# Optimization experiments

Measured on AMD Instinct MI355X. Metric: run time of the kernel, lower is better.

## Reference

```python
import jax, jax.numpy as jnp
import numpy as np

B, S, D = 2, 2048, 1024
E, H = 8, 2816  # hidden = 256*ceil(int(2*(4*1024)/3)/256) = 2816
TOP_K = 2


def setup_inputs() -> dict:
    key = jax.random.key(0)
    k0, k1, k2, k3, k4 = jax.random.split(key, 5)
    x = jax.random.normal(k0, (B, S, D), dtype=jnp.float32)
    wg = jax.random.normal(k1, (D, E), dtype=jnp.float32) * (D ** -0.5)
    w1 = jax.random.normal(k2, (E, D, H), dtype=jnp.float32) * 0.02  # gate proj
    w3 = jax.random.normal(k3, (E, D, H), dtype=jnp.float32) * 0.02  # up proj
    w2 = jax.random.normal(k4, (E, H, D), dtype=jnp.float32) * 0.02  # down proj
    return {"x": x, "wg": wg, "w1": w1, "w2": w2, "w3": w3}


def reference(x, wg, w1, w2, w3):
    Bb, Ss, Dd = x.shape
    Ee = w1.shape[0]
    xf = x.reshape(-1, Dd)                       # [T, D]
    logits = xf @ wg                              # [T, E]
    probs = jax.nn.softmax(logits, axis=-1)
    topk_p, topk_i = jax.lax.top_k(probs, TOP_K)  # [T, K]
    topk_p = topk_p / jnp.sum(topk_p, axis=-1, keepdims=True)
    # combine weight per (token, expert): sum over top-k slots
    cw = jnp.sum(jax.nn.one_hot(topk_i, Ee, dtype=xf.dtype) * topk_p[..., None], axis=1)  # [T, E]
    out = jnp.zeros_like(xf)
    for e in range(Ee):  # fixed small loop over experts
        h = jax.nn.silu(xf @ w1[e]) * (xf @ w3[e])   # [T, H] SwiGLU
        out = out + cw[:, e:e + 1] * (h @ w2[e])     # weighted combine
    return out.reshape(Bb, Ss, Dd)
```

## Files before the change

### kernel.cpp

```cpp
#include <hip/hip_runtime.h>
#include <hip/hip_bf16.h>

typedef unsigned short u16;
typedef __bf16 bf16_t;
typedef bf16_t bf16x8 __attribute__((ext_vector_type(8)));
typedef float f32x4 __attribute__((ext_vector_type(4)));

#define T_TOK 4096
#define DIM   1024
#define NEXP  8
#define HID   2816
#define CAP   16
#define DBUF  (128*32)

static __device__ __forceinline__ u16 f2b(float f) {
    __hip_bfloat16 h = __float2bfloat16(f);
    return *(u16*)&h;
}

static __device__ __forceinline__ void glds16(const u16* g, u16* l) {
    __builtin_amdgcn_global_load_lds((const __attribute__((address_space(1))) void*)g,
                                     (__attribute__((address_space(3))) void*)l, 16, 0, 0);
}

__global__ void k_gating(const float* __restrict__ X,
                         const float* __restrict__ WG,
                         int* __restrict__ cnt,
                         int* __restrict__ tok,
                         float* __restrict__ wt,
                         u16* __restrict__ Xbf)
{
    int wv   = threadIdx.x >> 6;
    int lane = threadIdx.x & 63;
    int t = blockIdx.x * 4 + wv;
    float l[NEXP];
#pragma unroll
    for (int e = 0; e < NEXP; ++e) l[e] = 0.f;
#pragma unroll
    for (int i = 0; i < DIM/64; ++i) {
        int d = i*64 + lane;
        float xv = X[(size_t)t*DIM + d];
        Xbf[(size_t)t*DIM + d] = f2b(xv);
        const float* wrow = WG + (size_t)d*NEXP;
        float4 wa = *(const float4*)wrow;
        float4 wb = *(const float4*)(wrow + 4);
        l[0] += xv*wa.x; l[1] += xv*wa.y; l[2] += xv*wa.z; l[3] += xv*wa.w;
        l[4] += xv*wb.x; l[5] += xv*wb.y; l[6] += xv*wb.z; l[7] += xv*wb.w;
    }
#pragma unroll
    for (int e = 0; e < NEXP; ++e) {
#pragma unroll
        for (int s = 32; s > 0; s >>= 1)
            l[e] += __shfl_xor(l[e], s, 64);
    }
    if (lane == 0) {
        int i1 = 0; float b1 = l[0];
#pragma unroll
        for (int e = 1; e < NEXP; ++e) if (l[e] > b1) { b1 = l[e]; i1 = e; }
        int i2 = -1; float b2 = 0.f;
#pragma unroll
        for (int e = 0; e < NEXP; ++e) {
            if (e == i1) continue;
            if (i2 < 0 || l[e] > b2) { b2 = l[e]; i2 = e; }
        }
        float p1 = 1.f / (1.f + __expf(b2 - b1));
        float p2 = 1.f - p1;
        int pos = atomicAdd(&cnt[i1], 1);
        tok[i1*T_TOK + pos] = t;  wt[i1*T_TOK + pos] = p1;
        pos = atomicAdd(&cnt[i2], 1);
        tok[i2*T_TOK + pos] = t;  wt[i2*T_TOK + pos] = p2;
    }
}

__global__ void k_compact(const int* __restrict__ cnt,
                          const int* __restrict__ tok, const float* __restrict__ wt,
                          int* __restrict__ ctok, float* __restrict__ cwt)
{
    int e = blockIdx.x;
    int off = 0;
    for (int i = 0; i < e; ++i) off += cnt[i];
    int n = cnt[e];
    for (int i = threadIdx.x; i < n; i += blockDim.x) {
        ctok[off + i] = tok[e*T_TOK + i];
        cwt [off + i] = wt [e*T_TOK + i];
    }
}

#define TS 72
__global__ void k_transpose_cast(const float* __restrict__ in, u16* __restrict__ out,
                                 int R, int C)
{
    __shared__ u16 tle[64*TS];
    size_t mb = (size_t)blockIdx.z * (size_t)R * C;
    int r0 = blockIdx.x * 64, c0 = blockIdx.y * 64;
    int tid = threadIdx.x;
    const float* I = in + mb + (size_t)r0*C + c0;
#pragma unroll
    for (int p = 0; p < 4; ++p) {
        int q = tid + p*256;
        int r = q >> 4, cc = (q & 15) * 4;
        float4 v = *(const float4*)&I[(size_t)r*C + cc];
        tle[(cc+0)*TS + r] = f2b(v.x);
        tle[(cc+1)*TS + r] = f2b(v.y);
        tle[(cc+2)*TS + r] = f2b(v.z);
        tle[(cc+3)*TS + r] = f2b(v.w);
    }
    __syncthreads();
    u16* O = out + mb + (size_t)c0*R + r0;
    int rc = tid & 7, oc = tid >> 3;
#pragma unroll
    for (int p = 0; p < 2; ++p) {
        int c = oc + p*32;
        *(uint4*)&O[(size_t)c*R + rc*8] = *(const uint4*)&tle[c*TS + rc*8];
    }
}

__global__ __launch_bounds__(256, 3) void k_gemm1(
    const u16* __restrict__ X, const u16* __restrict__ W1t, const u16* __restrict__ W3t,
    u16* __restrict__ Hbuf, const int* __restrict__ cnt, const int* __restrict__ ctok)
{
    __shared__ u16 As[2*DBUF];
    __shared__ u16 Bs[2*DBUF];
    __shared__ int tokLds[128];

    const int bid = blockIdx.x;
    const int e   = bid & 7;
    const int q   = bid >> 3;
    const int mt0 = q & (CAP-1);
    const int col = q >> 4;
    const int ne  = cnt[e];
    const int ntile = (ne + 127) >> 7;
    if (mt0 >= ntile) return;
    int off = 0;
    for (int i = 0; i < e; ++i) off += cnt[i];
    const int h0 = col * 64;

    const int tid = threadIdx.x, wave = tid >> 6, lane = tid & 63;
    const int wr = wave >> 1, wc = wave & 1;
    const int quad = lane >> 4, lr = lane & 15;
    const int lrow = lane >> 2;
    const int swk  = ((lane & 3) ^ ((lane >> 3) & 3)) * 8;
    const int jx   = (quad ^ ((lr >> 1) & 3)) * 8;

    const size_t wb = (size_t)e * HID * DIM;
    const u16* w1g = W1t + wb + (size_t)(h0 + wave*16 + lrow)*DIM + swk;
    const u16* w3g = W3t + wb + (size_t)(h0 + wave*16 + lrow)*DIM + swk;
    u16* aL0 = &As[(wave*16)*32];
    u16* aL1 = &As[(64 + wave*16)*32];
    u16* bL0 = &Bs[(wave*16)*32];
    u16* bL1 = &Bs[(64 + wave*16)*32];

#define G1_STAGE(K, OFS)              \
    glds16(ag0 + (K), aL0 + (OFS));   \
    glds16(ag1 + (K), aL1 + (OFS));   \
    glds16(w1g + (K), bL0 + (OFS));   \
    glds16(w3g + (K), bL1 + (OFS));

#define G1_COMPUTE(OFS)                                                             \
    {                                                                               \
        bf16x8 af[4], b1[2], b3[2];                                                 \
        _Pragma("unroll")                                                           \
        for (int m = 0; m < 4; ++m)                                                 \
            af[m] = *(const bf16x8*)&As[(OFS) + (wr*64 + m*16 + lr)*32 + jx];       \
        _Pragma("unroll")                                                           \
        for (int n = 0; n < 2; ++n) {                                               \
            b1[n] = *(const bf16x8*)&Bs[(OFS) + (wc*32 + n*16 + lr)*32 + jx];       \
            b3[n] = *(const bf16x8*)&Bs[(OFS) + (64 + wc*32 + n*16 + lr)*32 + jx];  \
        }                                                                           \
        __builtin_amdgcn_s_setprio(1);                                              \
        _Pragma("unroll")                                                           \
        for (int m = 0; m < 4; ++m)                                                 \
            _Pragma("unroll")                                                       \
            for (int n = 0; n < 2; ++n) {                                           \
                a1[m][n] = __builtin_amdgcn_mfma_f32_16x16x32_bf16(af[m], b1[n], a1[m][n], 0, 0, 0); \
                a3[m][n] = __builtin_amdgcn_mfma_f32_16x16x32_bf16(af[m], b3[n], a3[m][n], 0, 0, 0); \
            }                                                                       \
        __builtin_amdgcn_s_setprio(0);                                              \
    }

    for (int tile = mt0; tile < ntile; tile += CAP) {
        const int m0 = tile << 7;
        int nvalid = ne - m0; if (nvalid > 128) nvalid = 128;

        __syncthreads();
        if (tid < 128) {
            int i = (tid < nvalid) ? tid : (nvalid - 1);
            tokLds[tid] = ctok[off + m0 + i];
        }
        __syncthreads();
        const u16* ag0 = X + (size_t)tokLds[wave*16 + lrow]*DIM + swk;
        const u16* ag1 = X + (size_t)tokLds[64 + wave*16 + lrow]*DIM + swk;

        f32x4 a1[4][2], a3[4][2];
#pragma unroll
        for (int m = 0; m < 4; ++m)
#pragma unroll
            for (int n = 0; n < 2; ++n) {
                a1[m][n] = (f32x4){0.f,0.f,0.f,0.f};
                a3[m][n] = (f32x4){0.f,0.f,0.f,0.f};
            }

        G1_STAGE(0, 0)

        for (int k0 = 0; k0 < DIM; k0 += 64) {
            G1_STAGE(k0 + 32, DBUF)
            asm volatile("s_waitcnt vmcnt(4)" ::: "memory");
            __builtin_amdgcn_s_barrier();
            G1_COMPUTE(0)
            asm volatile("s_waitcnt lgkmcnt(0)" ::: "memory");
            __builtin_amdgcn_s_barrier();
            if (k0 + 64 < DIM) {
                G1_STAGE(k0 + 64, 0)
                asm volatile("s_waitcnt vmcnt(4)" ::: "memory");
            } else {
                asm volatile("s_waitcnt vmcnt(0)" ::: "memory");
            }
            __builtin_amdgcn_s_barrier();
            G1_COMPUTE(DBUF)
            asm volatile("s_waitcnt lgkmcnt(0)" ::: "memory");
            __builtin_amdgcn_s_barrier();
        }

#pragma unroll
        for (int m = 0; m < 4; ++m) {
            int mb_ = wr*64 + m*16 + quad*4;
#pragma unroll
            for (int rr = 0; rr < 4; ++rr) {
                int mm = mb_ + rr;
                if (mm >= nvalid) continue;
                u16* hrow = Hbuf + (size_t)(off + m0 + mm)*HID + h0 + wc*32 + lr;
#pragma unroll
                for (int n = 0; n < 2; ++n) {
                    float g = a1[m][n][rr];
                    float u = a3[m][n][rr];
                    hrow[n*16] = f2b((g / (1.f + __expf(-g))) * u);
                }
            }
        }
    }
#undef G1_STAGE
#undef G1_COMPUTE
}

__global__ __launch_bounds__(256, 3) void k_gemm2(
    const u16* __restrict__ Hbuf, const u16* __restrict__ W2t,
    float* __restrict__ outf, const int* __restrict__ cnt,
    const int* __restrict__ ctok, const float* __restrict__ cwt)
{
    __shared__ u16 As[2*DBUF];
    __shared__ u16 Bs[2*DBUF];
    __shared__ int   tLds[128];
    __shared__ float wLds[128];

    const int bid = blockIdx.x;
    const int e   = bid & 7;
    const int q   = bid >> 3;
    const int mt0 = q & (CAP-1);
    const int r2  = q >> 4;
    const int zk  = r2 & 1;
    const int d0  = (r2 >> 1) * 128;
    const int ne  = cnt[e];
    const int ntile = (ne + 127) >> 7;
    if (mt0 >= ntile) return;
    int off = 0;
    for (int i = 0; i < e; ++i) off += cnt[i];
    const int kb = zk * (HID/2);

    const int tid = threadIdx.x, wave = tid >> 6, lane = tid & 63;
    const int wr = wave >> 1, wc = wave & 1;
    const int quad = lane >> 4, lr = lane & 15;
    const int lrow = lane >> 2;
    const int swk  = ((lane & 3) ^ ((lane >> 3) & 3)) * 8;
    const int jx   = (quad ^ ((lr >> 1) & 3)) * 8;

    const size_t w2b = (size_t)e * DIM * HID;
    const u16* bg0 = W2t + w2b + (size_t)(d0 + wave*16 + lrow)*HID + kb + swk;
    const u16* bg1 = bg0 + (size_t)64*HID;
    u16* aL0 = &As[(wave*16)*32];
    u16* aL1 = &As[(64 + wave*16)*32];
    u16* bL0 = &Bs[(wave*16)*32];
    u16* bL1 = &Bs[(64 + wave*16)*32];

#define G2_STAGE(K, OFS)              \
    glds16(ag0 + (K), aL0 + (OFS));   \
    glds16(ag1 + (K), aL1 + (OFS));   \
    glds16(bg0 + (K), bL0 + (OFS));   \
    glds16(bg1 + (K), bL1 + (OFS));

#define G2_COMPUTE(OFS)                                                             \
    {                                                                               \
        bf16x8 af[4], bb[4];                                                        \
        _Pragma("unroll")                                                           \
        for (int m = 0; m < 4; ++m)                                                 \
            af[m] = *(const bf16x8*)&As[(OFS) + (wr*64 + m*16 + lr)*32 + jx];       \
        _Pragma("unroll")                                                           \
        for (int n = 0; n < 4; ++n)                                                 \
            bb[n] = *(const bf16x8*)&Bs[(OFS) + (wc*64 + n*16 + lr)*32 + jx];       \
        __builtin_amdgcn_s_setprio(1);                                              \
        _Pragma("unroll")                                                           \
        for (int m = 0; m < 4; ++m)                                                 \
            _Pragma("unroll")                                                       \
            for (int n = 0; n < 4; ++n)                                             \
                acc[m][n] = __builtin_amdgcn_mfma_f32_16x16x32_bf16(af[m], bb[n], acc[m][n], 0, 0, 0); \
        __builtin_amdgcn_s_setprio(0);                                              \
    }

    for (int tile = mt0; tile < ntile; tile += CAP) {
        const int m0 = tile << 7;
        int nvalid = ne - m0; if (nvalid > 128) nvalid = 128;

        __syncthreads();
        if (tid < 128) {
            int i = (tid < nvalid) ? tid : (nvalid - 1);
            tLds[tid] = ctok[off + m0 + i];
            wLds[tid] = cwt [off + m0 + i];
        }
        __syncthreads();
        int ar0 = wave*16 + lrow;      if (ar0 >= nvalid) ar0 = nvalid - 1;
        int ar1 = 64 + wave*16 + lrow; if (ar1 >= nvalid) ar1 = nvalid - 1;
        const u16* ag0 = Hbuf + (size_t)(off + m0 + ar0)*HID + kb + swk;
        const u16* ag1 = Hbuf + (size_t)(off + m0 + ar1)*HID + kb + swk;

        f32x4 acc[4][4];
#pragma unroll
        for (int a = 0; a < 4; ++a)
#pragma unroll
            for (int b = 0; b < 4; ++b) acc[a][b] = (f32x4){0.f,0.f,0.f,0.f};

        G2_STAGE(0, 0)

        for (int k0 = 0; k0 < HID/2; k0 += 64) {
            G2_STAGE(k0 + 32, DBUF)
            asm volatile("s_waitcnt vmcnt(4)" ::: "memory");
            __builtin_amdgcn_s_barrier();
            G2_COMPUTE(0)
            asm volatile("s_waitcnt lgkmcnt(0)" ::: "memory");
            __builtin_amdgcn_s_barrier();
            if (k0 + 64 < HID/2) {
                G2_STAGE(k0 + 64, 0)
                asm volatile("s_waitcnt vmcnt(4)" ::: "memory");
            } else {
                asm volatile("s_waitcnt vmcnt(0)" ::: "memory");
            }
            __builtin_amdgcn_s_barrier();
            G2_COMPUTE(DBUF)
            asm volatile("s_waitcnt lgkmcnt(0)" ::: "memory");
            __builtin_amdgcn_s_barrier();
        }

#pragma unroll
        for (int m = 0; m < 4; ++m) {
            int mb_ = wr*64 + m*16 + quad*4;
#pragma unroll
            for (int rr = 0; rr < 4; ++rr) {
                int mm = mb_ + rr;
                if (mm >= nvalid) continue;
                float wr_ = wLds[mm];
                float* orow = outf + (size_t)tLds[mm]*DIM + d0 + wc*64 + lr;
#pragma unroll
                for (int n = 0; n < 4; ++n)
                    atomicAdd(&orow[n*16], acc[m][n][rr] * wr_);
            }
        }
    }
#undef G2_STAGE
#undef G2_COMPUTE
}

extern "C" void kernel_launch(void* const* d_in, const int* in_sizes, int n_in,
                              void* d_out, int out_size, void* d_ws, size_t ws_size,
                              hipStream_t stream)
{
    const float* x  = (const float*)d_in[0];
    const float* wg = (const float*)d_in[1];
    const float* w1 = (const float*)d_in[2];
    const float* w2 = (const float*)d_in[3];
    const float* w3 = (const float*)d_in[4];
    float* outf = (float*)d_out;

    char* ws = (char*)d_ws;
    int*   cnt  = (int*)  (ws);
    int*   tok  = (int*)  (ws + 256);
    float* wt   = (float*)(ws + 131328);
    int*   ctok = (int*)  (ws + 262400);
    float* cwt  = (float*)(ws + 295168);
    u16*   Xbf  = (u16*)  (ws + 327936);
    u16*   Hbuf = (u16*)  (ws + 8716544);
    u16*   W1t  = (u16*)  (ws + 54853888);
    u16*   W3t  = (u16*)  (ws + 100991232);
    u16*   W2t  = (u16*)  (ws + 147128576);

    hipMemsetAsync(cnt, 0, 256, stream);
    hipMemsetAsync(outf, 0, (size_t)T_TOK*DIM*sizeof(float), stream);

    k_transpose_cast<<<dim3(DIM/64, HID/64, NEXP), 256, 0, stream>>>(w1, W1t, DIM, HID);
    k_transpose_cast<<<dim3(DIM/64, HID/64, NEXP), 256, 0, stream>>>(w3, W3t, DIM, HID);
    k_transpose_cast<<<dim3(HID/64, DIM/64, NEXP), 256, 0, stream>>>(w2, W2t, HID, DIM);

    k_gating<<<T_TOK/4, 256, 0, stream>>>(x, wg, cnt, tok, wt, Xbf);
    k_compact<<<NEXP, 256, 0, stream>>>(cnt, tok, wt, ctok, cwt);

    k_gemm1<<<NEXP*(HID/64)*CAP, 256, 0, stream>>>(Xbf, W1t, W3t, Hbuf, cnt, ctok);
    k_gemm2<<<NEXP*CAP*2*(DIM/128), 256, 0, stream>>>(Hbuf, W2t, outf, cnt, ctok, cwt);
}
```

Measured before the change: 663.8 us.

## Deepen GEMM LDS pipeline to four stages and swizzle transpose LDS

Both expert GEMM kernels move from a 2-slot double buffer to a 4-slot ring that keeps three K-slices of async global->LDS loads in flight, with explicit vmcnt waits and a drained epilogue. This is meant to hide more global memory latency behind the MFMA work. The cost is twice the LDS per block, so launch bounds drop from 3 to 2 blocks per CU, which lowers occupancy. The transpose-cast kernel also gets an XOR swizzle on its LDS tile to cut bank conflicts.

```diff
diff --git a/kernel.cpp b/kernel.cpp
--- a/kernel.cpp
+++ b/kernel.cpp
@@ -99,11 +99,12 @@
     for (int p = 0; p < 4; ++p) {
         int q = tid + p*256;
         int r = q >> 4, cc = (q & 15) * 4;
+        int rw = r ^ ((q & 7) << 3);
         float4 v = *(const float4*)&I[(size_t)r*C + cc];
-        tle[(cc+0)*TS + r] = f2b(v.x);
-        tle[(cc+1)*TS + r] = f2b(v.y);
-        tle[(cc+2)*TS + r] = f2b(v.z);
-        tle[(cc+3)*TS + r] = f2b(v.w);
+        tle[(cc+0)*TS + rw] = f2b(v.x);
+        tle[(cc+1)*TS + rw] = f2b(v.y);
+        tle[(cc+2)*TS + rw] = f2b(v.z);
+        tle[(cc+3)*TS + rw] = f2b(v.w);
     }
     __syncthreads();
     u16* O = out + mb + (size_t)c0*R + r0;
@@ -111,16 +112,17 @@
 #pragma unroll
     for (int p = 0; p < 2; ++p) {
         int c = oc + p*32;
-        *(uint4*)&O[(size_t)c*R + rc*8] = *(const uint4*)&tle[c*TS + rc*8];
-    }
-}
-
-__global__ __launch_bounds__(256, 3) void k_gemm1(
+        int rs = rc ^ ((c >> 2) & 7);
+        *(uint4*)&O[(size_t)c*R + rc*8] = *(const uint4*)&tle[c*TS + rs*8];
+    }
+}
+
+__global__ __launch_bounds__(256, 2) void k_gemm1(
     const u16* __restrict__ X, const u16* __restrict__ W1t, const u16* __restrict__ W3t,
     u16* __restrict__ Hbuf, const int* __restrict__ cnt, const int* __restrict__ ctok)
 {
-    __shared__ u16 As[2*DBUF];
-    __shared__ u16 Bs[2*DBUF];
+    __shared__ u16 As[4*DBUF];
+    __shared__ u16 Bs[4*DBUF];
     __shared__ int tokLds[128];
 
     const int bid = blockIdx.x;
@@ -150,11 +152,12 @@
     u16* bL0 = &Bs[(wave*16)*32];
     u16* bL1 = &Bs[(64 + wave*16)*32];
 
-#define G1_STAGE(K, OFS)              \
-    glds16(ag0 + (K), aL0 + (OFS));   \
-    glds16(ag1 + (K), aL1 + (OFS));   \
-    glds16(w1g + (K), bL0 + (OFS));   \
-    glds16(w3g + (K), bL1 + (OFS));
+#define G1_STAGE(S, SLOT)                         \
+    {   int _k = (S)*32;                          \
+        glds16(ag0 + _k, aL0 + (SLOT)*DBUF);      \
+        glds16(ag1 + _k, aL1 + (SLOT)*DBUF);      \
+        glds16(w1g + _k, bL0 + (SLOT)*DBUF);      \
+        glds16(w3g + _k, bL1 + (SLOT)*DBUF);  }
 
 #define G1_COMPUTE(OFS)                                                             \
     {                                                                               \
@@ -201,25 +204,42 @@
             }
 
         G1_STAGE(0, 0)
-
-        for (int k0 = 0; k0 < DIM; k0 += 64) {
-            G1_STAGE(k0 + 32, DBUF)
-            asm volatile("s_waitcnt vmcnt(4)" ::: "memory");
-            __builtin_amdgcn_s_barrier();
-            G1_COMPUTE(0)
-            asm volatile("s_waitcnt lgkmcnt(0)" ::: "memory");
-            __builtin_amdgcn_s_barrier();
-            if (k0 + 64 < DIM) {
-                G1_STAGE(k0 + 64, 0)
-                asm volatile("s_waitcnt vmcnt(4)" ::: "memory");
-            } else {
-                asm volatile("s_waitcnt vmcnt(0)" ::: "memory");
+        G1_STAGE(1, 1)
+        G1_STAGE(2, 2)
+
+        for (int j = 0; j < 32/4 - 1; ++j) {
+#pragma unroll
+            for (int t = 0; t < 4; ++t) {
+                const int i = 4*j + t;
+                G1_STAGE(i + 3, (t + 3) & 3)
+                asm volatile("s_waitcnt vmcnt(12)" ::: "memory");
+                __builtin_amdgcn_s_barrier();
+                G1_COMPUTE(t*DBUF)
+                asm volatile("s_waitcnt lgkmcnt(0)" ::: "memory");
+                __builtin_amdgcn_s_barrier();
             }
-            __builtin_amdgcn_s_barrier();
-            G1_COMPUTE(DBUF)
-            asm volatile("s_waitcnt lgkmcnt(0)" ::: "memory");
-            __builtin_amdgcn_s_barrier();
-        }
+        }
+        G1_STAGE(31, 3)
+        asm volatile("s_waitcnt vmcnt(12)" ::: "memory");
+        __builtin_amdgcn_s_barrier();
+        G1_COMPUTE(0*DBUF)
+        asm volatile("s_waitcnt lgkmcnt(0)" ::: "memory");
+        __builtin_amdgcn_s_barrier();
+        asm volatile("s_waitcnt vmcnt(8)" ::: "memory");
+        __builtin_amdgcn_s_barrier();
+        G1_COMPUTE(1*DBUF)
+        asm volatile("s_waitcnt lgkmcnt(0)" ::: "memory");
+        __builtin_amdgcn_s_barrier();
+        asm volatile("s_waitcnt vmcnt(4)" ::: "memory");
+        __builtin_amdgcn_s_barrier();
+        G1_COMPUTE(2*DBUF)
+        asm volatile("s_waitcnt lgkmcnt(0)" ::: "memory");
+        __builtin_amdgcn_s_barrier();
+        asm volatile("s_waitcnt vmcnt(0)" ::: "memory");
+        __builtin_amdgcn_s_barrier();
+        G1_COMPUTE(3*DBUF)
+        asm volatile("s_waitcnt lgkmcnt(0)" ::: "memory");
+        __builtin_amdgcn_s_barrier();
 
 #pragma unroll
         for (int m = 0; m < 4; ++m) {
@@ -242,13 +262,13 @@
 #undef G1_COMPUTE
 }
 
-__global__ __launch_bounds__(256, 3) void k_gemm2(
+__global__ __launch_bounds__(256, 2) void k_gemm2(
     const u16* __restrict__ Hbuf, const u16* __restrict__ W2t,
     float* __restrict__ outf, const int* __restrict__ cnt,
     const int* __restrict__ ctok, const float* __restrict__ cwt)
 {
-    __shared__ u16 As[2*DBUF];
-    __shared__ u16 Bs[2*DBUF];
+    __shared__ u16 As[4*DBUF];
+    __shared__ u16 Bs[4*DBUF];
     __shared__ int   tLds[128];
     __shared__ float wLds[128];
 
@@ -281,11 +301,12 @@
     u16* bL0 = &Bs[(wave*16)*32];
     u16* bL1 = &Bs[(64 + wave*16)*32];
 
-#define G2_STAGE(K, OFS)              \
-    glds16(ag0 + (K), aL0 + (OFS));   \
-    glds16(ag1 + (K), aL1 + (OFS));   \
-    glds16(bg0 + (K), bL0 + (OFS));   \
-    glds16(bg1 + (K), bL1 + (OFS));
+#define G2_STAGE(S, SLOT)                         \
+    {   int _k = (S)*32;                          \
+        glds16(ag0 + _k, aL0 + (SLOT)*DBUF);      \
+        glds16(ag1 + _k, aL1 + (SLOT)*DBUF);      \
+        glds16(bg0 + _k, bL0 + (SLOT)*DBUF);      \
+        glds16(bg1 + _k, bL1 + (SLOT)*DBUF);  }
 
 #define G2_COMPUTE(OFS)                                                             \
     {                                                                               \
@@ -328,25 +349,42 @@
             for (int b = 0; b < 4; ++b) acc[a][b] = (f32x4){0.f,0.f,0.f,0.f};
 
         G2_STAGE(0, 0)
-
-        for (int k0 = 0; k0 < HID/2; k0 += 64) {
-            G2_STAGE(k0 + 32, DBUF)
-            asm volatile("s_waitcnt vmcnt(4)" ::: "memory");
-            __builtin_amdgcn_s_barrier();
-            G2_COMPUTE(0)
-            asm volatile("s_waitcnt lgkmcnt(0)" ::: "memory");
-            __builtin_amdgcn_s_barrier();
-            if (k0 + 64 < HID/2) {
-                G2_STAGE(k0 + 64, 0)
-                asm volatile("s_waitcnt vmcnt(4)" ::: "memory");
-            } else {
-                asm volatile("s_waitcnt vmcnt(0)" ::: "memory");
+        G2_STAGE(1, 1)
+        G2_STAGE(2, 2)
+
+        for (int j = 0; j < 44/4 - 1; ++j) {
+#pragma unroll
+            for (int t = 0; t < 4; ++t) {
+                const int i = 4*j + t;
+                G2_STAGE(i + 3, (t + 3) & 3)
+                asm volatile("s_waitcnt vmcnt(12)" ::: "memory");
+                __builtin_amdgcn_s_barrier();
+                G2_COMPUTE(t*DBUF)
+                asm volatile("s_waitcnt lgkmcnt(0)" ::: "memory");
+                __builtin_amdgcn_s_barrier();
             }
-            __builtin_amdgcn_s_barrier();
-            G2_COMPUTE(DBUF)
-            asm volatile("s_waitcnt lgkmcnt(0)" ::: "memory");
-            __builtin_amdgcn_s_barrier();
-        }
+        }
+        G2_STAGE(43, 3)
+        asm volatile("s_waitcnt vmcnt(12)" ::: "memory");
+        __builtin_amdgcn_s_barrier();
+        G2_COMPUTE(0*DBUF)
+        asm volatile("s_waitcnt lgkmcnt(0)" ::: "memory");
+        __builtin_amdgcn_s_barrier();
+        asm volatile("s_waitcnt vmcnt(8)" ::: "memory");
+        __builtin_amdgcn_s_barrier();
+        G2_COMPUTE(1*DBUF)
+        asm volatile("s_waitcnt lgkmcnt(0)" ::: "memory");
+        __builtin_amdgcn_s_barrier();
+        asm volatile("s_waitcnt vmcnt(4)" ::: "memory");
+        __builtin_amdgcn_s_barrier();
+        G2_COMPUTE(2*DBUF)
+        asm volatile("s_waitcnt lgkmcnt(0)" ::: "memory");
+        __builtin_amdgcn_s_barrier();
+        asm volatile("s_waitcnt vmcnt(0)" ::: "memory");
+        __builtin_amdgcn_s_barrier();
+        G2_COMPUTE(3*DBUF)
+        asm volatile("s_waitcnt lgkmcnt(0)" ::: "memory");
+        __builtin_amdgcn_s_barrier();
 
 #pragma unroll
         for (int m = 0; m < 4; ++m) {
```

After: 681.1 us. 1.03x slower.

## Double N-tile width in expert GEMMs and swizzle transpose LDS writes

Applied to the files above, without the earlier changes.

Both expert GEMM kernels now compute twice as many output columns per block (128 hidden columns for gate/up, 256 output dims for down). This halves the grid and raises the MFMA work per loaded A fragment. Accumulator registers and LDS usage double, so launch bounds drop from 3 to 2 blocks per SM. The weight transpose-cast kernel also XOR-swizzles its LDS tile indices to cut bank conflicts on the scattered writes.

```diff
diff --git a/kernel.cpp b/kernel.cpp
--- a/kernel.cpp
+++ b/kernel.cpp
@@ -11,7 +11,8 @@
 #define NEXP  8
 #define HID   2816
 #define CAP   16
-#define DBUF  (128*32)
+#define ASZ   (128*32)
+#define BSZ   (256*32)
 
 static __device__ __forceinline__ u16 f2b(float f) {
     __hip_bfloat16 h = __float2bfloat16(f);
@@ -99,11 +100,12 @@
     for (int p = 0; p < 4; ++p) {
         int q = tid + p*256;
         int r = q >> 4, cc = (q & 15) * 4;
+        int rw = r ^ ((q & 7) << 3);
         float4 v = *(const float4*)&I[(size_t)r*C + cc];
-        tle[(cc+0)*TS + r] = f2b(v.x);
-        tle[(cc+1)*TS + r] = f2b(v.y);
-        tle[(cc+2)*TS + r] = f2b(v.z);
-        tle[(cc+3)*TS + r] = f2b(v.w);
+        tle[(cc+0)*TS + rw] = f2b(v.x);
+        tle[(cc+1)*TS + rw] = f2b(v.y);
+        tle[(cc+2)*TS + rw] = f2b(v.z);
+        tle[(cc+3)*TS + rw] = f2b(v.w);
     }
     __syncthreads();
     u16* O = out + mb + (size_t)c0*R + r0;
@@ -111,16 +113,17 @@
 #pragma unroll
     for (int p = 0; p < 2; ++p) {
         int c = oc + p*32;
-        *(uint4*)&O[(size_t)c*R + rc*8] = *(const uint4*)&tle[c*TS + rc*8];
-    }
-}
-
-__global__ __launch_bounds__(256, 3) void k_gemm1(
+        int rs = rc ^ ((c >> 2) & 7);
+        *(uint4*)&O[(size_t)c*R + rc*8] = *(const uint4*)&tle[c*TS + rs*8];
+    }
+}
+
+__global__ __launch_bounds__(256, 2) void k_gemm1(
     const u16* __restrict__ X, const u16* __restrict__ W1t, const u16* __restrict__ W3t,
     u16* __restrict__ Hbuf, const int* __restrict__ cnt, const int* __restrict__ ctok)
 {
-    __shared__ u16 As[2*DBUF];
-    __shared__ u16 Bs[2*DBUF];
+    __shared__ u16 As[2*ASZ];
+    __shared__ u16 Bs[2*BSZ];
     __shared__ int tokLds[128];
 
     const int bid = blockIdx.x;
@@ -133,7 +136,7 @@
     if (mt0 >= ntile) return;
     int off = 0;
     for (int i = 0; i < e; ++i) off += cnt[i];
-    const int h0 = col * 64;
+    const int h0 = col << 7;
 
     const int tid = threadIdx.x, wave = tid >> 6, lane = tid & 63;
     const int wr = wave >> 1, wc = wave & 1;
@@ -143,35 +146,33 @@
     const int jx   = (quad ^ ((lr >> 1) & 3)) * 8;
 
     const size_t wb = (size_t)e * HID * DIM;
-    const u16* w1g = W1t + wb + (size_t)(h0 + wave*16 + lrow)*DIM + swk;
-    const u16* w3g = W3t + wb + (size_t)(h0 + wave*16 + lrow)*DIM + swk;
-    u16* aL0 = &As[(wave*16)*32];
-    u16* aL1 = &As[(64 + wave*16)*32];
-    u16* bL0 = &Bs[(wave*16)*32];
-    u16* bL1 = &Bs[(64 + wave*16)*32];
-
-#define G1_STAGE(K, OFS)              \
-    glds16(ag0 + (K), aL0 + (OFS));   \
-    glds16(ag1 + (K), aL1 + (OFS));   \
-    glds16(w1g + (K), bL0 + (OFS));   \
-    glds16(w3g + (K), bL1 + (OFS));
-
-#define G1_COMPUTE(OFS)                                                             \
+    const u16* w1g = W1t + wb + (size_t)(h0 + wave*32 + lrow)*DIM + swk;
+    const u16* w3g = W3t + wb + (size_t)(h0 + wave*32 + lrow)*DIM + swk;
+
+#define G1_STAGE(K, OA, OB)                                   \
+    glds16(ag0 + (K), As + (OA) + wave*1024);                 \
+    glds16(ag1 + (K), As + (OA) + wave*1024 + 512);           \
+    glds16(w1g + (K), Bs + (OB) + wave*1024);                 \
+    glds16(w1g + 16*DIM + (K), Bs + (OB) + wave*1024 + 512);  \
+    glds16(w3g + (K), Bs + (OB) + 4096 + wave*1024);          \
+    glds16(w3g + 16*DIM + (K), Bs + (OB) + 4096 + wave*1024 + 512);
+
+#define G1_COMPUTE(OA, OB)                                                          \
     {                                                                               \
-        bf16x8 af[4], b1[2], b3[2];                                                 \
+        bf16x8 af[4], b1[4], b3[4];                                                 \
         _Pragma("unroll")                                                           \
         for (int m = 0; m < 4; ++m)                                                 \
-            af[m] = *(const bf16x8*)&As[(OFS) + (wr*64 + m*16 + lr)*32 + jx];       \
-        _Pragma("unroll")                                                           \
-        for (int n = 0; n < 2; ++n) {                                               \
-            b1[n] = *(const bf16x8*)&Bs[(OFS) + (wc*32 + n*16 + lr)*32 + jx];       \
-            b3[n] = *(const bf16x8*)&Bs[(OFS) + (64 + wc*32 + n*16 + lr)*32 + jx];  \
+            af[m] = *(const bf16x8*)&As[(OA) + (wr*64 + m*16 + lr)*32 + jx];        \
+        _Pragma("unroll")                                                           \
+        for (int n = 0; n < 4; ++n) {                                               \
+            b1[n] = *(const bf16x8*)&Bs[(OB) + (wc*64 + n*16 + lr)*32 + jx];        \
+            b3[n] = *(const bf16x8*)&Bs[(OB) + 4096 + (wc*64 + n*16 + lr)*32 + jx]; \
         }                                                                           \
         __builtin_amdgcn_s_setprio(1);                                              \
         _Pragma("unroll")                                                           \
         for (int m = 0; m < 4; ++m)                                                 \
             _Pragma("unroll")                                                       \
-            for (int n = 0; n < 2; ++n) {                                           \
+            for (int n = 0; n < 4; ++n) {                                           \
                 a1[m][n] = __builtin_amdgcn_mfma_f32_16x16x32_bf16(af[m], b1[n], a1[m][n], 0, 0, 0); \
                 a3[m][n] = __builtin_amdgcn_mfma_f32_16x16x32_bf16(af[m], b3[n], a3[m][n], 0, 0, 0); \
             }                                                                       \
@@ -188,35 +189,35 @@
             tokLds[tid] = ctok[off + m0 + i];
         }
         __syncthreads();
-        const u16* ag0 = X + (size_t)tokLds[wave*16 + lrow]*DIM + swk;
-        const u16* ag1 = X + (size_t)tokLds[64 + wave*16 + lrow]*DIM + swk;
-
-        f32x4 a1[4][2], a3[4][2];
+        const u16* ag0 = X + (size_t)tokLds[wave*32 + lrow]*DIM + swk;
+        const u16* ag1 = X + (size_t)tokLds[wave*32 + 16 + lrow]*DIM + swk;
+
+        f32x4 a1[4][4], a3[4][4];
 #pragma unroll
         for (int m = 0; m < 4; ++m)
 #pragma unroll
-            for (int n = 0; n < 2; ++n) {
+            for (int n = 0; n < 4; ++n) {
                 a1[m][n] = (f32x4){0.f,0.f,0.f,0.f};
                 a3[m][n] = (f32x4){0.f,0.f,0.f,0.f};
             }
 
-        G1_STAGE(0, 0)
+        G1_STAGE(0, 0, 0)
 
         for (int k0 = 0; k0 < DIM; k0 += 64) {
-            G1_STAGE(k0 + 32, DBUF)
-            asm volatile("s_waitcnt vmcnt(4)" ::: "memory");
-            __builtin_amdgcn_s_barrier();
-            G1_COMPUTE(0)
+            G1_STAGE(k0 + 32, ASZ, BSZ)
+            asm volatile("s_waitcnt vmcnt(6)" ::: "memory");
+            __builtin_amdgcn_s_barrier();
+            G1_COMPUTE(0, 0)
             asm volatile("s_waitcnt lgkmcnt(0)" ::: "memory");
             __builtin_amdgcn_s_barrier();
             if (k0 + 64 < DIM) {
-                G1_STAGE(k0 + 64, 0)
-                asm volatile("s_waitcnt vmcnt(4)" ::: "memory");
+                G1_STAGE(k0 + 64, 0, 0)
+                asm volatile("s_waitcnt vmcnt(6)" ::: "memory");
             } else {
                 asm volatile("s_waitcnt vmcnt(0)" ::: "memory");
             }
             __builtin_amdgcn_s_barrier();
-            G1_COMPUTE(DBUF)
+            G1_COMPUTE(ASZ, BSZ)
             asm volatile("s_waitcnt lgkmcnt(0)" ::: "memory");
             __builtin_amdgcn_s_barrier();
         }
@@ -228,9 +229,9 @@
             for (int rr = 0; rr < 4; ++rr) {
                 int mm = mb_ + rr;
                 if (mm >= nvalid) continue;
-                u16* hrow = Hbuf + (size_t)(off + m0 + mm)*HID + h0 + wc*32 + lr;
-#pragma unroll
-                for (int n = 0; n < 2; ++n) {
+                u16* hrow = Hbuf + (size_t)(off + m0 + mm)*HID + h0 + wc*64 + lr;
+#pragma unroll
+                for (int n = 0; n < 4; ++n) {
                     float g = a1[m][n][rr];
                     float u = a3[m][n][rr];
                     hrow[n*16] = f2b((g / (1.f + __expf(-g))) * u);
@@ -242,13 +243,13 @@
 #undef G1_COMPUTE
 }
 
-__global__ __launch_bounds__(256, 3) void k_gemm2(
+__global__ __launch_bounds__(256, 2) void k_gemm2(
     const u16* __restrict__ Hbuf, const u16* __restrict__ W2t,
     float* __restrict__ outf, const int* __restrict__ cnt,
     const int* __restrict__ ctok, const float* __restrict__ cwt)
 {
-    __shared__ u16 As[2*DBUF];
-    __shared__ u16 Bs[2*DBUF];
+    __shared__ u16 As[2*ASZ];
+    __shared__ u16 Bs[2*BSZ];
     __shared__ int   tLds[128];
     __shared__ float wLds[128];
 
@@ -258,7 +259,7 @@
     const int mt0 = q & (CAP-1);
     const int r2  = q >> 4;
     const int zk  = r2 & 1;
-    const int d0  = (r2 >> 1) * 128;
+    const int d0  = (r2 >> 1) << 8;
     const int ne  = cnt[e];
     const int ntile = (ne + 127) >> 7;
     if (mt0 >= ntile) return;
@@ -274,33 +275,30 @@
     const int jx   = (quad ^ ((lr >> 1) & 3)) * 8;
 
     const size_t w2b = (size_t)e * DIM * HID;
-    const u16* bg0 = W2t + w2b + (size_t)(d0 + wave*16 + lrow)*HID + kb + swk;
-    const u16* bg1 = bg0 + (size_t)64*HID;
-    u16* aL0 = &As[(wave*16)*32];
-    u16* aL1 = &As[(64 + wave*16)*32];
-    u16* bL0 = &Bs[(wave*16)*32];
-    u16* bL1 = &Bs[(64 + wave*16)*32];
-
-#define G2_STAGE(K, OFS)              \
-    glds16(ag0 + (K), aL0 + (OFS));   \
-    glds16(ag1 + (K), aL1 + (OFS));   \
-    glds16(bg0 + (K), bL0 + (OFS));   \
-    glds16(bg1 + (K), bL1 + (OFS));
-
-#define G2_COMPUTE(OFS)                                                             \
+    const u16* bg = W2t + w2b + (size_t)(d0 + wave*64 + lrow)*HID + kb + swk;
+
+#define G2_STAGE(K, OA, OB)                                   \
+    glds16(ag0 + (K), As + (OA) + wave*1024);                 \
+    glds16(ag1 + (K), As + (OA) + wave*1024 + 512);           \
+    glds16(bg + (K),          Bs + (OB) + wave*2048);         \
+    glds16(bg + 16*HID + (K), Bs + (OB) + wave*2048 + 512);   \
+    glds16(bg + 32*HID + (K), Bs + (OB) + wave*2048 + 1024);  \
+    glds16(bg + 48*HID + (K), Bs + (OB) + wave*2048 + 1536);
+
+#define G2_COMPUTE(OA, OB)                                                          \
     {                                                                               \
-        bf16x8 af[4], bb[4];                                                        \
+        bf16x8 af[4], bb[8];                                                        \
         _Pragma("unroll")                                                           \
         for (int m = 0; m < 4; ++m)                                                 \
-            af[m] = *(const bf16x8*)&As[(OFS) + (wr*64 + m*16 + lr)*32 + jx];       \
-        _Pragma("unroll")                                                           \
-        for (int n = 0; n < 4; ++n)                                                 \
-            bb[n] = *(const bf16x8*)&Bs[(OFS) + (wc*64 + n*16 + lr)*32 + jx];       \
+            af[m] = *(const bf16x8*)&As[(OA) + (wr*64 + m*16 + lr)*32 + jx];        \
+        _Pragma("unroll")                                                           \
+        for (int n = 0; n < 8; ++n)                                                 \
+            bb[n] = *(const bf16x8*)&Bs[(OB) + (wc*128 + n*16 + lr)*32 + jx];       \
         __builtin_amdgcn_s_setprio(1);                                              \
         _Pragma("unroll")                                                           \
         for (int m = 0; m < 4; ++m)                                                 \
             _Pragma("unroll")                                                       \
-            for (int n = 0; n < 4; ++n)                                             \
+            for (int n = 0; n < 8; ++n)                                             \
                 acc[m][n] = __builtin_amdgcn_mfma_f32_16x16x32_bf16(af[m], bb[n], acc[m][n], 0, 0, 0); \
         __builtin_amdgcn_s_setprio(0);                                              \
     }
@@ -316,34 +314,34 @@
             wLds[tid] = cwt [off + m0 + i];
         }
         __syncthreads();
-        int ar0 = wave*16 + lrow;      if (ar0 >= nvalid) ar0 = nvalid - 1;
-        int ar1 = 64 + wave*16 + lrow; if (ar1 >= nvalid) ar1 = nvalid - 1;
+        int ar0 = wave*32 + lrow;      if (ar0 >= nvalid) ar0 = nvalid - 1;
+        int ar1 = wave*32 + 16 + lrow; if (ar1 >= nvalid) ar1 = nvalid - 1;
         const u16* ag0 = Hbuf + (size_t)(off + m0 + ar0)*HID + kb + swk;
         const u16* ag1 = Hbuf + (size_t)(off + m0 + ar1)*HID + kb + swk;
 
-        f32x4 acc[4][4];
+        f32x4 acc[4][8];
 #pragma unroll
         for (int a = 0; a < 4; ++a)
 #pragma unroll
-            for (int b = 0; b < 4; ++b) acc[a][b] = (f32x4){0.f,0.f,0.f,0.f};
-
-        G2_STAGE(0, 0)
+            for (int b = 0; b < 8; ++b) acc[a][b] = (f32x4){0.f,0.f,0.f,0.f};
+
+        G2_STAGE(0, 0, 0)
 
         for (int k0 = 0; k0 < HID/2; k0 += 64) {
-            G2_STAGE(k0 + 32, DBUF)
-            asm volatile("s_waitcnt vmcnt(4)" ::: "memory");
-            __builtin_amdgcn_s_barrier();
-            G2_COMPUTE(0)
+            G2_STAGE(k0 + 32, ASZ, BSZ)
+            asm volatile("s_waitcnt vmcnt(6)" ::: "memory");
+            __builtin_amdgcn_s_barrier();
+            G2_COMPUTE(0, 0)
             asm volatile("s_waitcnt lgkmcnt(0)" ::: "memory");
             __builtin_amdgcn_s_barrier();
             if (k0 + 64 < HID/2) {
-                G2_STAGE(k0 + 64, 0)
-                asm volatile("s_waitcnt vmcnt(4)" ::: "memory");
+                G2_STAGE(k0 + 64, 0, 0)
+                asm volatile("s_waitcnt vmcnt(6)" ::: "memory");
             } else {
                 asm volatile("s_waitcnt vmcnt(0)" ::: "memory");
             }
             __builtin_amdgcn_s_barrier();
-            G2_COMPUTE(DBUF)
+            G2_COMPUTE(ASZ, BSZ)
             asm volatile("s_waitcnt lgkmcnt(0)" ::: "memory");
             __builtin_amdgcn_s_barrier();
         }
@@ -356,9 +354,9 @@
                 int mm = mb_ + rr;
                 if (mm >= nvalid) continue;
                 float wr_ = wLds[mm];
-                float* orow = outf + (size_t)tLds[mm]*DIM + d0 + wc*64 + lr;
-#pragma unroll
-                for (int n = 0; n < 4; ++n)
+                float* orow = outf + (size_t)tLds[mm]*DIM + d0 + wc*128 + lr;
+#pragma unroll
+                for (int n = 0; n < 8; ++n)
                     atomicAdd(&orow[n*16], acc[m][n][rr] * wr_);
             }
         }
@@ -400,6 +398,6 @@
     k_gating<<<T_TOK/4, 256, 0, stream>>>(x, wg, cnt, tok, wt, Xbf);
     k_compact<<<NEXP, 256, 0, stream>>>(cnt, tok, wt, ctok, cwt);
 
-    k_gemm1<<<NEXP*(HID/64)*CAP, 256, 0, stream>>>(Xbf, W1t, W3t, Hbuf, cnt, ctok);
-    k_gemm2<<<NEXP*CAP*2*(DIM/128), 256, 0, stream>>>(Hbuf, W2t, outf, cnt, ctok, cwt);
-}
+    k_gemm1<<<NEXP*(HID/128)*CAP, 256, 0, stream>>>(Xbf, W1t, W3t, Hbuf, cnt, ctok);
+    k_gemm2<<<NEXP*CAP*2*(DIM/256), 256, 0, stream>>>(Hbuf, W2t, outf, cnt, ctok, cwt);
+}
```

After: 687.2 us. 1.04x slower.
